# Kernel optimization log

Measured on AMD Instinct MI355X. Metric: run time of the kernel, lower is better.

Reference implementation:

```python
import jax, jax.numpy as jnp
import numpy as np

DIM = 96
GS = 8          # group_size (window side)
CS = 64         # cluster_size
TOPK = 3


def setup_inputs() -> dict:
    key = jax.random.key(0)
    ks = jax.random.split(key, 12)
    B, C, H, W = 4, DIM, 256, 256
    s = 0.02
    return {
        "x":      jax.random.normal(ks[0], (B, C, H, W), jnp.float32),
        "Wq":     jax.random.normal(ks[1], (C, C), jnp.float32) * s,
        "bq":     jnp.zeros((C,), jnp.float32),
        "Wk":     jax.random.normal(ks[2], (C, C), jnp.float32) * s,
        "bk":     jnp.zeros((C,), jnp.float32),
        "Wv":     jax.random.normal(ks[3], (C, C), jnp.float32) * s,
        "bv":     jnp.zeros((C,), jnp.float32),
        "Wp":     jax.random.normal(ks[4], (C, C), jnp.float32) * s,
        "bp":     jnp.zeros((C,), jnp.float32),
        "lepe_w": jax.random.normal(ks[5], (C, 1, 3, 3), jnp.float32) * s,
        "lepe_b": jnp.zeros((C,), jnp.float32),
    }


def _dwconv3x3(x, w, b):
    # x: [N,C,h,w], w: [C,1,3,3] depthwise
    y = jax.lax.conv_general_dilated(
        x, w, window_strides=(1, 1), padding=((1, 1), (1, 1)),
        feature_group_count=x.shape[1],
        dimension_numbers=("NCHW", "OIHW", "NCHW"))
    return y + b[None, :, None, None]


def reference(x, Wq, bq, Wk, bk, Wv, bv, Wp, bp, lepe_w, lepe_b):
    B, C, H, W = x.shape
    gh, gw = H // GS, W // GS
    N = B * gh * gw                      # total windows
    itr = N // CS                        # number of clusters
    P = GS * GS                          # tokens per window
    scale = C ** (-0.5)

    # adaptive_max_pool2d to (gh,gw) == non-overlapping max pool of stride GS
    dsx = x.reshape(B, C, gh, GS, gw, GS).max(axis=(3, 5))        # [B,C,gh,gw]
    dsx = dsx.transpose(0, 2, 3, 1).reshape(itr, CS, C)           # [itr,CS,C]

    # global window-similarity with two-stage topk (faithful to nested loop)
    sim = jnp.einsum('icd,jed->icje', dsx, dsx)                   # [itr,CS,itr,CS]
    blk_s, blk_i = jax.lax.top_k(sim, TOPK)                       # [itr,CS,itr,TOPK]
    blk_gi = blk_i + (jnp.arange(itr) * CS)[None, None, :, None]  # global indices
    cat_s = blk_s.reshape(itr, CS, itr * TOPK)
    cat_i = blk_gi.reshape(itr, CS, itr * TOPK)
    fin_s, fi = jax.lax.top_k(cat_s, TOPK)                        # [itr,CS,TOPK]
    fin_i = jnp.take_along_axis(cat_i, fi, axis=-1)
    sim_score = fin_s.reshape(N, TOPK)
    sim_index = fin_i.reshape(N, TOPK)

    # window partition: [N, P, C]
    xw = x.transpose(0, 2, 3, 1).reshape(B, gh, GS, gw, GS, C)
    xw = xw.transpose(0, 1, 3, 2, 4, 5).reshape(N, P, C)

    # weighted combination of topk neighbor windows
    w = jax.nn.softmax(sim_score, axis=-1)                        # [N,TOPK]
    neighbors = xw[sim_index]                                     # [N,TOPK,P,C]
    context = jnp.einsum('nk,nkpc->npc', w, neighbors)            # [N,P,C]

    # windowed cross attention: Q from x windows, K/V from gathered context
    q = xw @ Wq + bq
    k = context @ Wk + bk
    v = context @ Wv + bv

    # lepe: depthwise conv positional bias on x windows
    x_img = xw.transpose(0, 2, 1).reshape(N, C, GS, GS)
    lepe = _dwconv3x3(x_img, lepe_w, lepe_b).reshape(N, C, P).transpose(0, 2, 1)

    attn = jax.nn.softmax(jnp.einsum('npc,nqc->npq', q, k) * scale, axis=-1)
    out = jnp.einsum('npq,nqc->npc', attn, v) + lepe
    out = out @ Wp + bp                                           # [N,P,C]

    # reverse window partition -> [B,C,H,W]
    out = out.reshape(B, gh, gw, GS, GS, C)
    out = out.transpose(0, 5, 1, 3, 2, 4).reshape(B, C, H, W)
    return out
```

## Files before the change

kernel.cpp:

```cpp
#include <hip/hip_runtime.h>

typedef __attribute__((ext_vector_type(8))) short  short8;
typedef __attribute__((ext_vector_type(4))) float  f32x4;
typedef __attribute__((ext_vector_type(4))) unsigned int uint4v;
typedef __attribute__((ext_vector_type(2))) unsigned int uint2v;

#define NEG_INF (-3.402823466e38f)

__device__ __forceinline__ unsigned short bfbits(float f) {
    unsigned u = __builtin_bit_cast(unsigned, f);
    u += 0x7fffu + ((u >> 16) & 1u);
    return (unsigned short)(u >> 16);
}
__device__ __forceinline__ unsigned pk_bf16(float lo, float hi) {
    return (unsigned)bfbits(lo) | ((unsigned)bfbits(hi) << 16);
}
__device__ __forceinline__ float lofp(unsigned u) {
    return __builtin_bit_cast(float, u << 16);
}
__device__ __forceinline__ float hifp(unsigned u) {
    return __builtin_bit_cast(float, u & 0xffff0000u);
}
__device__ __forceinline__ float bf2f(short x) {
    return __builtin_bit_cast(float, ((unsigned)(unsigned short)x) << 16);
}

__device__ __forceinline__ void ins3(float (&tv)[3], int (&ti)[3], float v, int ci)
{
    if (v > tv[0] || (v == tv[0] && ci < ti[0])) {
        tv[2] = tv[1]; ti[2] = ti[1];
        tv[1] = tv[0]; ti[1] = ti[0];
        tv[0] = v;     ti[0] = ci;
    } else if (v > tv[1] || (v == tv[1] && ci < ti[1])) {
        tv[2] = tv[1]; ti[2] = ti[1];
        tv[1] = v;     ti[1] = ci;
    } else if (v > tv[2] || (v == tv[2] && ci < ti[2])) {
        tv[2] = v;     ti[2] = ci;
    }
}

__global__ __launch_bounds__(256) void k_pool(const float* __restrict__ x,
                                              float* __restrict__ dsxT)
{
    int gid = blockIdx.x * 256 + threadIdx.x;
    int c = gid >> 12;
    int n = gid & 4095;
    int b = n >> 10, i = (n >> 5) & 31, j = n & 31;
    const float* p = x + (((size_t)(b * 96 + c)) << 16) + i * 2048 + j * 8;
    float4 m0 = *(const float4*)p;
    float4 m1 = *(const float4*)(p + 4);
    #pragma unroll
    for (int r = 1; r < 8; ++r) {
        float4 a0 = *(const float4*)(p + r * 256);
        float4 a1 = *(const float4*)(p + r * 256 + 4);
        m0.x = fmaxf(m0.x, a0.x); m0.y = fmaxf(m0.y, a0.y);
        m0.z = fmaxf(m0.z, a0.z); m0.w = fmaxf(m0.w, a0.w);
        m1.x = fmaxf(m1.x, a1.x); m1.y = fmaxf(m1.y, a1.y);
        m1.z = fmaxf(m1.z, a1.z); m1.w = fmaxf(m1.w, a1.w);
    }
    float m = fmaxf(fmaxf(fmaxf(m0.x, m0.y), fmaxf(m0.z, m0.w)),
                    fmaxf(fmaxf(m1.x, m1.y), fmaxf(m1.z, m1.w)));
    dsxT[c * 4096 + n] = m;
}

__global__ __launch_bounds__(768) void k_cast(const float* __restrict__ x,
                                              unsigned short* __restrict__ xwg,
                                              unsigned short* __restrict__ dsxH,
                                              unsigned short* __restrict__ dsxM,
                                              unsigned short* __restrict__ dsxL)
{
    int n = ((blockIdx.x & 7) << 9) | (blockIdx.x >> 3);
    int t = threadIdx.x;
    int cg = t >> 6, p = t & 63;
    int b = n >> 10, i = (n >> 5) & 31, j = n & 31;
    int h = i * 8 + (p >> 3), w = j * 8 + (p & 7);
    size_t base = (((size_t)(b * 96 + 8 * cg)) << 16) + (size_t)(h * 256 + w);
    float v[8];
    #pragma unroll
    for (int jj = 0; jj < 8; ++jj) v[jj] = x[base + (((size_t)jj) << 16)];
    uint4v pk;
    #pragma unroll
    for (int jj = 0; jj < 4; ++jj) pk[jj] = pk_bf16(v[2 * jj], v[2 * jj + 1]);
    *(uint4v*)&xwg[(size_t)n * 6144 + p * 96 + 8 * cg] = pk;
    #pragma unroll
    for (int jj = 0; jj < 8; ++jj) {
        float m = v[jj];
        #pragma unroll
        for (int d = 1; d < 64; d <<= 1) m = fmaxf(m, __shfl_xor(m, d, 64));
        if (p == 0) {
            unsigned short hb = bfbits(m);
            float r1 = m - __builtin_bit_cast(float, ((unsigned)hb) << 16);
            unsigned short mb = bfbits(r1);
            float r2 = r1 - __builtin_bit_cast(float, ((unsigned)mb) << 16);
            dsxH[n * 96 + 8 * cg + jj] = hb;
            dsxM[n * 96 + 8 * cg + jj] = mb;
            dsxL[n * 96 + 8 * cg + jj] = bfbits(r2);
        }
    }
}

__global__ __launch_bounds__(256) void k_sim(const float* __restrict__ dsxT,
                                             float* __restrict__ pv,
                                             int* __restrict__ pi)
{
    __shared__ __align__(16) float qt[32 * 128];
    __shared__ __align__(16) float ct[32 * 144];
    int t = threadIdx.x;
    int qti = blockIdx.x >> 4;
    int ch  = blockIdx.x & 15;
    int ty = t >> 4, tx = t & 15;
    int qb = qti * 128;

    float tv[8][3]; int ti[8][3];
    #pragma unroll
    for (int a = 0; a < 8; ++a)
        #pragma unroll
        for (int k = 0; k < 3; ++k) { tv[a][k] = NEG_INF; ti[a][k] = 0x7fffffff; }

    #pragma unroll
    for (int pass = 0; pass < 2; ++pass) {
        int cb = ch * 256 + pass * 128;
        float acc[8][8];
        #pragma unroll
        for (int a = 0; a < 8; ++a)
            #pragma unroll
            for (int e = 0; e < 8; ++e) acc[a][e] = 0.f;

        for (int kc = 0; kc < 3; ++kc) {
            __syncthreads();
            #pragma unroll
            for (int f4 = 0; f4 < 4; ++f4) {
                int f = t + f4 * 256;
                int kk = f >> 5, cq = f & 31;
                *(float4*)&qt[kk * 128 + 4 * cq] =
                    *(const float4*)&dsxT[(kc * 32 + kk) * 4096 + qb + 4 * cq];
                *(float4*)&ct[kk * 144 + 4 * cq + 4 * (cq >> 3)] =
                    *(const float4*)&dsxT[(kc * 32 + kk) * 4096 + cb + 4 * cq];
            }
            __syncthreads();
            #pragma unroll 2
            for (int kk = 0; kk < 32; ++kk) {
                float4 q0 = *(float4*)&qt[kk * 128 + 8 * ty];
                float4 q1 = *(float4*)&qt[kk * 128 + 8 * ty + 4];
                int e0 = 8 * tx, e1 = 8 * tx + 4;
                float4 c0 = *(float4*)&ct[kk * 144 + e0 + 4 * (e0 >> 5)];
                float4 c1 = *(float4*)&ct[kk * 144 + e1 + 4 * (e1 >> 5)];
                float qv[8] = {q0.x, q0.y, q0.z, q0.w, q1.x, q1.y, q1.z, q1.w};
                float cv[8] = {c0.x, c0.y, c0.z, c0.w, c1.x, c1.y, c1.z, c1.w};
                #pragma unroll
                for (int a = 0; a < 8; ++a)
                    #pragma unroll
                    for (int e = 0; e < 8; ++e)
                        acc[a][e] = fmaf(qv[a], cv[e], acc[a][e]);
            }
        }
        #pragma unroll
        for (int e = 0; e < 8; ++e) {
            int ci = cb + 8 * tx + e;
            #pragma unroll
            for (int a = 0; a < 8; ++a) ins3(tv[a], ti[a], acc[a][e], ci);
        }
    }

    #pragma unroll
    for (int d = 1; d < 16; d <<= 1) {
        #pragma unroll
        for (int a = 0; a < 8; ++a) {
            float ov[3]; int oi[3];
            #pragma unroll
            for (int k = 0; k < 3; ++k) {
                ov[k] = __shfl_xor(tv[a][k], d, 16);
                oi[k] = __shfl_xor(ti[a][k], d, 16);
            }
            #pragma unroll
            for (int k = 0; k < 3; ++k) ins3(tv[a], ti[a], ov[k], oi[k]);
        }
    }
    if (tx == 0) {
        #pragma unroll
        for (int a = 0; a < 8; ++a) {
            int nq = qti * 128 + 8 * ty + a;
            #pragma unroll
            for (int k = 0; k < 3; ++k) {
                pv[nq * 48 + ch * 3 + k] = tv[a][k];
                pi[nq * 48 + ch * 3 + k] = ti[a][k];
            }
        }
    }
}

__global__ __launch_bounds__(256) void k_sim_bf(const unsigned short* __restrict__ dsxH,
                                                const unsigned short* __restrict__ dsxM,
                                                const unsigned short* __restrict__ dsxL,
                                                int* __restrict__ pi)
{
    int t = threadIdx.x;
    int qti = blockIdx.x >> 4;
    int ch  = blockIdx.x & 15;
    int lane = t & 63, wv = t >> 6;
    int l15 = lane & 15, quad = lane >> 4;
    int cb = ch * 256;

    #pragma unroll
    for (int a2 = 0; a2 < 2; ++a2) {
        int at = wv * 2 + a2;
        int qrow = qti * 128 + at * 16 + l15;
        short8 aH[3], aM[3], aL[3];
        #pragma unroll
        for (int ks = 0; ks < 3; ++ks) {
            aH[ks] = *(const short8*)&dsxH[qrow * 96 + ks * 32 + quad * 8];
            aM[ks] = *(const short8*)&dsxM[qrow * 96 + ks * 32 + quad * 8];
            aL[ks] = *(const short8*)&dsxL[qrow * 96 + ks * 32 + quad * 8];
        }
        float tv[4][3]; int ti[4][3];
        #pragma unroll
        for (int r = 0; r < 4; ++r)
            #pragma unroll
            for (int k = 0; k < 3; ++k) { tv[r][k] = NEG_INF; ti[r][k] = 0x7fffffff; }

        for (int bt = 0; bt < 16; ++bt) {
            int crow = cb + bt * 16 + l15;
            f32x4 c  = {0.f, 0.f, 0.f, 0.f};
            f32x4 c2 = {0.f, 0.f, 0.f, 0.f};
            #pragma unroll
            for (int ks = 0; ks < 3; ++ks) {
                short8 bH = *(const short8*)&dsxH[crow * 96 + ks * 32 + quad * 8];
                short8 bM = *(const short8*)&dsxM[crow * 96 + ks * 32 + quad * 8];
                short8 bL = *(const short8*)&dsxL[crow * 96 + ks * 32 + quad * 8];
                c  = __builtin_amdgcn_mfma_f32_16x16x32_bf16(aH[ks], bH, c,  0, 0, 0);
                c2 = __builtin_amdgcn_mfma_f32_16x16x32_bf16(aH[ks], bM, c2, 0, 0, 0);
                c2 = __builtin_amdgcn_mfma_f32_16x16x32_bf16(aM[ks], bH, c2, 0, 0, 0);
                c2 = __builtin_amdgcn_mfma_f32_16x16x32_bf16(aM[ks], bM, c2, 0, 0, 0);
                c2 = __builtin_amdgcn_mfma_f32_16x16x32_bf16(aH[ks], bL, c2, 0, 0, 0);
                c2 = __builtin_amdgcn_mfma_f32_16x16x32_bf16(aL[ks], bH, c2, 0, 0, 0);
            }
            #pragma unroll
            for (int r = 0; r < 4; ++r)
                ins3(tv[r], ti[r], c[r] + c2[r], cb + bt * 16 + l15);
        }
        #pragma unroll
        for (int d = 1; d < 16; d <<= 1) {
            #pragma unroll
            for (int r = 0; r < 4; ++r) {
                float ov[3]; int oi[3];
                #pragma unroll
                for (int k = 0; k < 3; ++k) {
                    ov[k] = __shfl_xor(tv[r][k], d, 16);
                    oi[k] = __shfl_xor(ti[r][k], d, 16);
                }
                #pragma unroll
                for (int k = 0; k < 3; ++k) ins3(tv[r], ti[r], ov[k], oi[k]);
            }
        }
        if (l15 == 0) {
            #pragma unroll
            for (int r = 0; r < 4; ++r) {
                int nq = qti * 128 + at * 16 + quad * 4 + r;
                #pragma unroll
                for (int k = 0; k < 3; ++k)
                    pi[nq * 48 + ch * 3 + k] = ti[r][k];
            }
        }
    }
}

__global__ __launch_bounds__(256) void k_top3x(const unsigned short* __restrict__ dsxH,
                                               const unsigned short* __restrict__ dsxM,
                                               const unsigned short* __restrict__ dsxL,
                                               const int* __restrict__ pi,
                                               float* __restrict__ w3,
                                               int* __restrict__ i3)
{
    int t = threadIdx.x;
    int lane = t & 63, wv = t >> 6;
    int n = blockIdx.x * 4 + wv;
    int cand = (lane < 48) ? pi[n * 48 + lane] : 0;
    float s = 0.f;
    #pragma unroll
    for (int ck = 0; ck < 12; ++ck) {
        short8 qh = *(const short8*)&dsxH[n * 96 + ck * 8];
        short8 qm = *(const short8*)&dsxM[n * 96 + ck * 8];
        short8 ql = *(const short8*)&dsxL[n * 96 + ck * 8];
        short8 kh = *(const short8*)&dsxH[cand * 96 + ck * 8];
        short8 km = *(const short8*)&dsxM[cand * 96 + ck * 8];
        short8 kl = *(const short8*)&dsxL[cand * 96 + ck * 8];
        #pragma unroll
        for (int e = 0; e < 8; ++e) {
            float qv = (bf2f(qh[e]) + bf2f(qm[e])) + bf2f(ql[e]);
            float kv = (bf2f(kh[e]) + bf2f(km[e])) + bf2f(kl[e]);
            s = fmaf(qv, kv, s);
        }
    }
    float tv[3] = {NEG_INF, NEG_INF, NEG_INF};
    int   ti[3] = {0x7fffffff, 0x7fffffff, 0x7fffffff};
    if (lane < 48) { tv[0] = s; ti[0] = cand; }
    #pragma unroll
    for (int d = 1; d < 64; d <<= 1) {
        float ov[3]; int oi[3];
        #pragma unroll
        for (int k = 0; k < 3; ++k) {
            ov[k] = __shfl_xor(tv[k], d, 64);
            oi[k] = __shfl_xor(ti[k], d, 64);
        }
        #pragma unroll
        for (int k = 0; k < 3; ++k) ins3(tv, ti, ov[k], oi[k]);
    }
    if (lane == 0) {
        float e1 = expf(tv[1] - tv[0]);
        float e2 = expf(tv[2] - tv[0]);
        float inv = 1.f / (1.f + e1 + e2);
        w3[n * 3 + 0] = inv;
        w3[n * 3 + 1] = e1 * inv;
        w3[n * 3 + 2] = e2 * inv;
        i3[n * 3 + 0] = ti[0];
        i3[n * 3 + 1] = ti[1];
        i3[n * 3 + 2] = ti[2];
    }
}

__global__ __launch_bounds__(256) void k_topk(const float* __restrict__ pv,
                                              const int* __restrict__ pi,
                                              float* __restrict__ w3,
                                              int* __restrict__ i3)
{
    int n = blockIdx.x * 256 + threadIdx.x;
    float bv[3] = {NEG_INF, NEG_INF, NEG_INF};
    int   bi[3] = {0x7fffffff, 0x7fffffff, 0x7fffffff};
    for (int e = 0; e < 48; ++e)
        ins3(bv, bi, pv[n * 48 + e], pi[n * 48 + e]);
    float e1 = expf(bv[1] - bv[0]);
    float e2 = expf(bv[2] - bv[0]);
    float inv = 1.f / (1.f + e1 + e2);
    w3[n * 3 + 0] = inv;
    w3[n * 3 + 1] = e1 * inv;
    w3[n * 3 + 2] = e2 * inv;
    i3[n * 3 + 0] = bi[0];
    i3[n * 3 + 1] = bi[1];
    i3[n * 3 + 2] = bi[2];
}

__global__ __launch_bounds__(256) void k_prep(const float* __restrict__ Wq,
                                              const float* __restrict__ Wk,
                                              const float* __restrict__ Wv,
                                              const float* __restrict__ Wp,
                                              const float* __restrict__ lw,
                                              unsigned short* __restrict__ WtT,
                                              float* __restrict__ lwT)
{
    int g = blockIdx.x * 256 + threadIdx.x;
    if (g < 4608) {
        int w  = g / 1152;
        int co = (g % 1152) / 12;
        int cg = g % 12;
        const float* src = (w == 0) ? Wq : (w == 1) ? Wk : (w == 2) ? Wv : Wp;
        unsigned short* dst = WtT + w * 9216 + co * 96 + 8 * cg;
        #pragma unroll
        for (int j = 0; j < 8; ++j) dst[j] = bfbits(src[(8 * cg + j) * 96 + co]);
    } else if (g < 5472) {
        int i2 = g - 4608;
        int tap = i2 / 96, c = i2 % 96;
        lwT[tap * 96 + c] = lw[c * 9 + tap];
    }
}

__device__ __forceinline__ size_t win_off(int m)
{
    return (((size_t)(m >> 10) * 96) << 16) +
           (size_t)(((m >> 5) & 31) * 2048 + (m & 31) * 8);
}

__device__ __forceinline__ void gemm_g(const short8* af,
                                       const unsigned short* __restrict__ Wt,
                                       int l15, int quad, f32x4* acc)
{
    #pragma unroll
    for (int nt = 0; nt < 6; ++nt) {
        f32x4 c = {0.f, 0.f, 0.f, 0.f};
        #pragma unroll
        for (int ks = 0; ks < 3; ++ks) {
            short8 bf = *(const short8*)&Wt[(nt * 16 + l15) * 96 + ks * 32 + quad * 8];
            c = __builtin_amdgcn_mfma_f32_16x16x32_bf16(af[ks], bf, c, 0, 0, 0);
        }
        acc[nt] = c;
    }
}

template<bool XWG>
__global__ __attribute__((amdgpu_waves_per_eu(4, 4)))
__launch_bounds__(256) void k_attn(
    const float* __restrict__ x,
    const unsigned short* __restrict__ xwg,
    const unsigned short* __restrict__ WtT,
    const float* __restrict__ lwT,
    const float* __restrict__ bq, const float* __restrict__ bk,
    const float* __restrict__ bv, const float* __restrict__ bp,
    const float* __restrict__ lb,
    const float* __restrict__ w3, const int* __restrict__ i3,
    float* __restrict__ out)
{
    extern __shared__ __align__(16) unsigned short sm[];
    unsigned short* buf1 = sm;
    unsigned short* buf2 = sm + 6656;
    unsigned short* Vt   = sm + 13312;

    int t = threadIdx.x;
    int n = ((blockIdx.x & 7) << 9) | (blockIdx.x >> 3);
    int lane = t & 63, mt = t >> 6;
    int l15 = lane & 15, quad = lane >> 4;

    float wk0 = w3[n * 3 + 0], wk1 = w3[n * 3 + 1], wk2 = w3[n * 3 + 2];
    int   m0  = i3[n * 3 + 0], m1 = i3[n * 3 + 1], m2 = i3[n * 3 + 2];

    if (XWG) {
        #pragma unroll
        for (int it = 0; it < 3; ++it) {
            int g = it * 256 + t;
            int p = g / 12, cg = g % 12;
            int o = p * 96 + 8 * cg;
            uint4v sv = *(const uint4v*)&xwg[(size_t)n * 6144 + o];
            *(uint4v*)&buf1[p * 104 + 8 * cg] = sv;
            uint4v a0 = *(const uint4v*)&xwg[(size_t)m0 * 6144 + o];
            uint4v a1 = *(const uint4v*)&xwg[(size_t)m1 * 6144 + o];
            uint4v a2 = *(const uint4v*)&xwg[(size_t)m2 * 6144 + o];
            uint4v rs;
            #pragma unroll
            for (int e = 0; e < 4; ++e) {
                float lo = wk0 * lofp(a0[e]) + wk1 * lofp(a1[e]) + wk2 * lofp(a2[e]);
                float hi = wk0 * hifp(a0[e]) + wk1 * hifp(a1[e]) + wk2 * hifp(a2[e]);
                rs[e] = pk_bf16(lo, hi);
            }
            *(uint4v*)&buf2[p * 104 + 8 * cg] = rs;
        }
    } else {
        size_t so = win_off(n), o0 = win_off(m0), o1 = win_off(m1), o2 = win_off(m2);
        #pragma unroll
        for (int it = 0; it < 3; ++it) {
            int g = it * 256 + t;
            int p = g / 12, cg = g % 12;
            size_t po = (size_t)((p >> 3) * 256 + (p & 7));
            uint4v ra, rb;
            #pragma unroll
            for (int jj = 0; jj < 4; ++jj) {
                size_t clo = (((size_t)(8 * cg + 2 * jj)) << 16) + po;
                size_t chi = clo + ((size_t)1 << 16);
                ra[jj] = pk_bf16(x[so + clo], x[so + chi]);
                float blo = wk0 * x[o0 + clo] + wk1 * x[o1 + clo] + wk2 * x[o2 + clo];
                float bhi = wk0 * x[o0 + chi] + wk1 * x[o1 + chi] + wk2 * x[o2 + chi];
                rb[jj] = pk_bf16(blo, bhi);
            }
            *(uint4v*)&buf1[p * 104 + 8 * cg] = ra;
            *(uint4v*)&buf2[p * 104 + 8 * cg] = rb;
        }
    }
    __syncthreads();

    short8 af_a[3], af_b[3];
    int arow = (mt * 16 + l15) * 104;
    #pragma unroll
    for (int ks = 0; ks < 3; ++ks) {
        af_a[ks] = *(const short8*)&buf1[arow + ks * 32 + quad * 8];
        af_b[ks] = *(const short8*)&buf2[arow + ks * 32 + quad * 8];
    }
    unsigned Lp[12];
    {
        int rowp = mt * 16 + l15;
        int c0 = 24 * quad;
        int rr0 = rowp >> 3, ss0 = rowp & 7;
        float lac[24];
        #pragma unroll
        for (int q4 = 0; q4 < 6; ++q4) {
            float4 bb = *(const float4*)&lb[c0 + 4 * q4];
            lac[4 * q4] = bb.x; lac[4 * q4 + 1] = bb.y;
            lac[4 * q4 + 2] = bb.z; lac[4 * q4 + 3] = bb.w;
        }
        #pragma unroll
        for (int dr = -1; dr <= 1; ++dr) {
            int rr = rr0 + dr;
            if ((unsigned)rr >= 8u) continue;
            #pragma unroll
            for (int dss = -1; dss <= 1; ++dss) {
                int ss = ss0 + dss;
                if ((unsigned)ss >= 8u) continue;
                int pp = rr * 8 + ss;
                int tap = (dr + 1) * 3 + (dss + 1);
                const uint4v* ap = (const uint4v*)&buf1[pp * 104 + c0];
                uint4v av0 = ap[0], av1 = ap[1], av2 = ap[2];
                float wf[24];
                #pragma unroll
                for (int q4 = 0; q4 < 6; ++q4) {
                    float4 ww = *(const float4*)&lwT[tap * 96 + c0 + 4 * q4];
                    wf[4 * q4] = ww.x; wf[4 * q4 + 1] = ww.y;
                    wf[4 * q4 + 2] = ww.z; wf[4 * q4 + 3] = ww.w;
                }
                #pragma unroll
                for (int u = 0; u < 12; ++u) {
                    unsigned uu = (u < 4) ? av0[u] : (u < 8) ? av1[u - 4] : av2[u - 8];
                    lac[2 * u]     = fmaf(wf[2 * u],     lofp(uu), lac[2 * u]);
                    lac[2 * u + 1] = fmaf(wf[2 * u + 1], hifp(uu), lac[2 * u + 1]);
                }
            }
        }
        #pragma unroll
        for (int u = 0; u < 12; ++u) Lp[u] = pk_bf16(lac[2 * u], lac[2 * u + 1]);
    }
    __syncthreads();

    {
        f32x4 qa[6];
        gemm_g(af_a, WtT, l15, quad, qa);
        #pragma unroll
        for (int nt = 0; nt < 6; ++nt) {
            int col = nt * 16 + l15;
            float bb = bq[col];
            #pragma unroll
            for (int r = 0; r < 4; ++r)
                buf1[(mt * 16 + quad * 4 + r) * 104 + col] = bfbits(qa[nt][r] + bb);
        }
    }
    __builtin_amdgcn_sched_barrier(0);
    {
        f32x4 ka[6];
        gemm_g(af_b, WtT + 9216, l15, quad, ka);
        #pragma unroll
        for (int nt = 0; nt < 6; ++nt) {
            int col = nt * 16 + l15;
            float bb = bk[col];
            #pragma unroll
            for (int r = 0; r < 4; ++r)
                buf2[(mt * 16 + quad * 4 + r) * 104 + col] = bfbits(ka[nt][r] + bb);
        }
    }
    __builtin_amdgcn_sched_barrier(0);
    {
        f32x4 va[6];
        gemm_g(af_b, WtT + 18432, l15, quad, va);
        #pragma unroll
        for (int nt = 0; nt < 6; ++nt) {
            float bb = bv[nt * 16 + l15];
            uint2v pk;
            pk[0] = pk_bf16(va[nt][0] + bb, va[nt][1] + bb);
            pk[1] = pk_bf16(va[nt][2] + bb, va[nt][3] + bb);
            *(uint2v*)&Vt[(nt * 16 + l15) * 72 + mt * 16 + quad * 4] = pk;
        }
    }
    __syncthreads();

    float pr[4][4], inv4[4];
    {
        short8 qf[3];
        #pragma unroll
        for (int ks = 0; ks < 3; ++ks)
            qf[ks] = *(const short8*)&buf1[arow + ks * 32 + quad * 8];
        f32x4 sa[4];
        #pragma unroll
        for (int nt = 0; nt < 4; ++nt) {
            f32x4 c = {0.f, 0.f, 0.f, 0.f};
            #pragma unroll
            for (int ks = 0; ks < 3; ++ks) {
                short8 bf = *(const short8*)&buf2[(nt * 16 + l15) * 104 + ks * 32 + quad * 8];
                c = __builtin_amdgcn_mfma_f32_16x16x32_bf16(qf[ks], bf, c, 0, 0, 0);
            }
            sa[nt] = c;
        }
        const float scale = 0.10206207261596575f;
        #pragma unroll
        for (int r = 0; r < 4; ++r) {
            float mx = fmaxf(fmaxf(sa[0][r], sa[1][r]), fmaxf(sa[2][r], sa[3][r]));
            #pragma unroll
            for (int d = 1; d < 16; d <<= 1) mx = fmaxf(mx, __shfl_xor(mx, d, 16));
            float sum = 0.f;
            #pragma unroll
            for (int nt = 0; nt < 4; ++nt) {
                float e = __expf((sa[nt][r] - mx) * scale);
                pr[r][nt] = e; sum += e;
            }
            #pragma unroll
            for (int d = 1; d < 16; d <<= 1) sum += __shfl_xor(sum, d, 16);
            inv4[r] = 1.f / sum;
        }
    }
    __syncthreads();

    #pragma unroll
    for (int r = 0; r < 4; ++r) {
        #pragma unroll
        for (int nt = 0; nt < 4; ++nt)
            buf1[(mt * 16 + quad * 4 + r) * 104 + nt * 16 + l15] =
                bfbits(pr[r][nt] * inv4[r]);
    }
    {
        uint4v* lp = (uint4v*)&buf2[arow + 24 * quad];
        uint4v l0 = {Lp[0], Lp[1], Lp[2], Lp[3]};
        uint4v l1 = {Lp[4], Lp[5], Lp[6], Lp[7]};
        uint4v l2 = {Lp[8], Lp[9], Lp[10], Lp[11]};
        lp[0] = l0; lp[1] = l1; lp[2] = l2;
    }

    {
        short8 sf[2];
        sf[0] = *(const short8*)&buf1[arow + quad * 8];
        sf[1] = *(const short8*)&buf1[arow + 32 + quad * 8];
        f32x4 oa[6];
        #pragma unroll
        for (int nt = 0; nt < 6; ++nt) {
            f32x4 c = {0.f, 0.f, 0.f, 0.f};
            #pragma unroll
            for (int ks = 0; ks < 2; ++ks) {
                short8 bf = *(const short8*)&Vt[(nt * 16 + l15) * 72 + ks * 32 + quad * 8];
                c = __builtin_amdgcn_mfma_f32_16x16x32_bf16(sf[ks], bf, c, 0, 0, 0);
            }
            oa[nt] = c;
        }
        #pragma unroll
        for (int nt = 0; nt < 6; ++nt)
            #pragma unroll
            for (int r = 0; r < 4; ++r)
                buf1[(mt * 16 + quad * 4 + r) * 104 + nt * 16 + l15] = bfbits(oa[nt][r]);
    }

    {
        short8 of[3], lf[3];
        #pragma unroll
        for (int ks = 0; ks < 3; ++ks) {
            of[ks] = *(const short8*)&buf1[arow + ks * 32 + quad * 8];
            lf[ks] = *(const short8*)&buf2[arow + ks * 32 + quad * 8];
        }
        const unsigned short* Wp_ = WtT + 27648;
        int b = n >> 10, ii = (n >> 5) & 31, jj = n & 31;
        size_t pbase = (size_t)(ii * 2048 + jj * 8 + mt * 512 +
                                (quad >> 1) * 256 + (quad & 1) * 4);
        #pragma unroll
        for (int nt = 0; nt < 6; ++nt) {
            f32x4 c = {0.f, 0.f, 0.f, 0.f};
            #pragma unroll
            for (int ks = 0; ks < 3; ++ks) {
                short8 bf = *(const short8*)&Wp_[(nt * 16 + l15) * 96 + ks * 32 + quad * 8];
                c = __builtin_amdgcn_mfma_f32_16x16x32_bf16(of[ks], bf, c, 0, 0, 0);
                c = __builtin_amdgcn_mfma_f32_16x16x32_bf16(lf[ks], bf, c, 0, 0, 0);
            }
            int co = nt * 16 + l15;
            float bb = bp[co];
            float4 st;
            st.x = c[0] + bb; st.y = c[1] + bb; st.z = c[2] + bb; st.w = c[3] + bb;
            *(float4*)&out[(((size_t)(b * 96 + co)) << 16) + pbase] = st;
        }
    }
}

extern "C" void kernel_launch(void* const* d_in, const int* in_sizes, int n_in,
                              void* d_out, int out_size, void* d_ws, size_t ws_size,
                              hipStream_t stream)
{
    (void)in_sizes; (void)n_in; (void)out_size;
    const float* x  = (const float*)d_in[0];
    const float* Wq = (const float*)d_in[1];
    const float* bq = (const float*)d_in[2];
    const float* Wk = (const float*)d_in[3];
    const float* bk = (const float*)d_in[4];
    const float* Wv = (const float*)d_in[5];
    const float* bv = (const float*)d_in[6];
    const float* Wp = (const float*)d_in[7];
    const float* bp = (const float*)d_in[8];
    const float* lw = (const float*)d_in[9];
    const float* lb = (const float*)d_in[10];
    float* out = (float*)d_out;

    char* ws = (char*)d_ws;
    float* dsxT = (float*)ws;
    unsigned short* dsxH = (unsigned short*)ws;
    unsigned short* dsxM = (unsigned short*)(ws + 786432);
    unsigned short* dsxL = (unsigned short*)(ws + 1572864);
    float* pv   = (float*)(ws + 1572864);
    int*   pi   = (int*)  (ws + 2359296);
    float* w3   = (float*)(ws + 3145728);
    int*   i3   = (int*)  (ws + 3194880);
    unsigned short* WtT = (unsigned short*)(ws + 3244032);
    float* lwT  = (float*)(ws + 3317760);
    unsigned short* xwg = (unsigned short*)(ws + 3321344);
    bool use_xwg = (ws_size >= 53652992ull);

    (void)hipFuncSetAttribute(reinterpret_cast<const void*>(&k_attn<true>),
                        hipFuncAttributeMaxDynamicSharedMemorySize, 40448);
    (void)hipFuncSetAttribute(reinterpret_cast<const void*>(&k_attn<false>),
                        hipFuncAttributeMaxDynamicSharedMemorySize, 40448);

    k_prep<<<22, 256, 0, stream>>>(Wq, Wk, Wv, Wp, lw, WtT, lwT);
    if (use_xwg) {
        k_cast<<<4096, 768, 0, stream>>>(x, xwg, dsxH, dsxM, dsxL);
        k_sim_bf<<<512, 256, 0, stream>>>(dsxH, dsxM, dsxL, pi);
        k_top3x<<<1024, 256, 0, stream>>>(dsxH, dsxM, dsxL, pi, w3, i3);
        k_attn<true><<<4096, 256, 40448, stream>>>(x, xwg, WtT, lwT, bq, bk, bv, bp,
                                                   lb, w3, i3, out);
    } else {
        k_pool<<<1536, 256, 0, stream>>>(x, dsxT);
        k_sim<<<512, 256, 0, stream>>>(dsxT, pv, pi);
        k_topk<<<16, 256, 0, stream>>>(pv, pi, w3, i3);
        k_attn<false><<<4096, 256, 40448, stream>>>(x, nullptr, WtT, lwT, bq, bk, bv, bp,
                                                    lb, w3, i3, out);
    }
}
```

Measured before the change: 428.4 us.

## Stage similarity B tiles through double-buffered LDS and raise MFMA wave priority

The similarity kernel now has each block cover 64 query rows instead of 128 and launches twice as many blocks. The three bf16 key planes are staged cooperatively into a double-buffered shared-memory tile, with the next tile's global loads issued before the current tile's MFMAs. This replaces redundant per-wave global loads of B and overlaps them with compute. Separately, s_setprio is raised around the MFMA loops in the attention kernel to favour matrix-issuing waves, at the cost of an extra barrier per tile and more LDS use.

```diff
diff --git a/kernel.cpp b/kernel.cpp
--- a/kernel.cpp
+++ b/kernel.cpp
@@ -189,11 +189,12 @@
     }
 }
 
-__global__ __launch_bounds__(256) void k_sim_bf(const unsigned short* __restrict__ dsxH,
-                                                const unsigned short* __restrict__ dsxM,
-                                                const unsigned short* __restrict__ dsxL,
-                                                int* __restrict__ pi)
-{
+__global__ __launch_bounds__(256, 4) void k_sim_bf(const unsigned short* __restrict__ dsxH,
+                                                   const unsigned short* __restrict__ dsxM,
+                                                   const unsigned short* __restrict__ dsxL,
+                                                   int* __restrict__ pi)
+{
+    __shared__ __align__(16) unsigned short Bs[2][16 * 296];
     int t = threadIdx.x;
     int qti = blockIdx.x >> 4;
     int ch  = blockIdx.x & 15;
@@ -201,65 +202,103 @@
     int l15 = lane & 15, quad = lane >> 4;
     int cb = ch * 256;
 
-    #pragma unroll
-    for (int a2 = 0; a2 < 2; ++a2) {
-        int at = wv * 2 + a2;
-        int qrow = qti * 128 + at * 16 + l15;
-        short8 aH[3], aM[3], aL[3];
+    int qrow = qti * 64 + wv * 16 + l15;
+    short8 aH[3], aM[3], aL[3];
+    #pragma unroll
+    for (int ks = 0; ks < 3; ++ks) {
+        aH[ks] = *(const short8*)&dsxH[qrow * 96 + ks * 32 + quad * 8];
+        aM[ks] = *(const short8*)&dsxM[qrow * 96 + ks * 32 + quad * 8];
+        aL[ks] = *(const short8*)&dsxL[qrow * 96 + ks * 32 + quad * 8];
+    }
+
+    int ldsoff[3], goff[3];
+    const unsigned short* srcp[3];
+    #pragma unroll
+    for (int kc = 0; kc < 3; ++kc) {
+        int c = t + kc * 256;
+        int row = c / 36, w36 = c % 36;
+        int plane = w36 / 12, idx = w36 % 12;
+        ldsoff[kc] = row * 296 + plane * 96 + idx * 8;
+        goff[kc]   = row * 96 + idx * 8;
+        srcp[kc]   = (plane == 0) ? dsxH : (plane == 1) ? dsxM : dsxL;
+    }
+    bool third = (t < 64);
+
+    float tv[4][3]; int ti[4][3];
+    #pragma unroll
+    for (int r = 0; r < 4; ++r)
+        #pragma unroll
+        for (int k = 0; k < 3; ++k) { tv[r][k] = NEG_INF; ti[r][k] = 0x7fffffff; }
+
+    {
+        int base = cb * 96;
+        uint4v v0 = *(const uint4v*)&srcp[0][base + goff[0]];
+        uint4v v1 = *(const uint4v*)&srcp[1][base + goff[1]];
+        *(uint4v*)&Bs[0][ldsoff[0]] = v0;
+        *(uint4v*)&Bs[0][ldsoff[1]] = v1;
+        if (third) {
+            uint4v v2 = *(const uint4v*)&srcp[2][base + goff[2]];
+            *(uint4v*)&Bs[0][ldsoff[2]] = v2;
+        }
+    }
+    __syncthreads();
+
+    for (int st = 0; st < 16; ++st) {
+        int cur = st & 1;
+        uint4v p0, p1, p2;
+        if (st < 15) {
+            int base = (cb + (st + 1) * 16) * 96;
+            p0 = *(const uint4v*)&srcp[0][base + goff[0]];
+            p1 = *(const uint4v*)&srcp[1][base + goff[1]];
+            if (third) p2 = *(const uint4v*)&srcp[2][base + goff[2]];
+        }
+        f32x4 c = {0.f, 0.f, 0.f, 0.f};
+        f32x4 c2 = {0.f, 0.f, 0.f, 0.f};
         #pragma unroll
         for (int ks = 0; ks < 3; ++ks) {
-            aH[ks] = *(const short8*)&dsxH[qrow * 96 + ks * 32 + quad * 8];
-            aM[ks] = *(const short8*)&dsxM[qrow * 96 + ks * 32 + quad * 8];
-            aL[ks] = *(const short8*)&dsxL[qrow * 96 + ks * 32 + quad * 8];
-        }
-        float tv[4][3]; int ti[4][3];
+            int bo = l15 * 296 + ks * 32 + quad * 8;
+            short8 bH = *(const short8*)&Bs[cur][bo];
+            short8 bM = *(const short8*)&Bs[cur][bo + 96];
+            short8 bL = *(const short8*)&Bs[cur][bo + 192];
+            c  = __builtin_amdgcn_mfma_f32_16x16x32_bf16(aH[ks], bH, c,  0, 0, 0);
+            c2 = __builtin_amdgcn_mfma_f32_16x16x32_bf16(aH[ks], bM, c2, 0, 0, 0);
+            c2 = __builtin_amdgcn_mfma_f32_16x16x32_bf16(aM[ks], bH, c2, 0, 0, 0);
+            c2 = __builtin_amdgcn_mfma_f32_16x16x32_bf16(aM[ks], bM, c2, 0, 0, 0);
+            c2 = __builtin_amdgcn_mfma_f32_16x16x32_bf16(aH[ks], bL, c2, 0, 0, 0);
+            c2 = __builtin_amdgcn_mfma_f32_16x16x32_bf16(aL[ks], bH, c2, 0, 0, 0);
+        }
         #pragma unroll
         for (int r = 0; r < 4; ++r)
-            #pragma unroll
-            for (int k = 0; k < 3; ++k) { tv[r][k] = NEG_INF; ti[r][k] = 0x7fffffff; }
-
-        for (int bt = 0; bt < 16; ++bt) {
-            int crow = cb + bt * 16 + l15;
-            f32x4 c  = {0.f, 0.f, 0.f, 0.f};
-            f32x4 c2 = {0.f, 0.f, 0.f, 0.f};
-            #pragma unroll
-            for (int ks = 0; ks < 3; ++ks) {
-                short8 bH = *(const short8*)&dsxH[crow * 96 + ks * 32 + quad * 8];
-                short8 bM = *(const short8*)&dsxM[crow * 96 + ks * 32 + quad * 8];
-                short8 bL = *(const short8*)&dsxL[crow * 96 + ks * 32 + quad * 8];
-                c  = __builtin_amdgcn_mfma_f32_16x16x32_bf16(aH[ks], bH, c,  0, 0, 0);
-                c2 = __builtin_amdgcn_mfma_f32_16x16x32_bf16(aH[ks], bM, c2, 0, 0, 0);
-                c2 = __builtin_amdgcn_mfma_f32_16x16x32_bf16(aM[ks], bH, c2, 0, 0, 0);
-                c2 = __builtin_amdgcn_mfma_f32_16x16x32_bf16(aM[ks], bM, c2, 0, 0, 0);
-                c2 = __builtin_amdgcn_mfma_f32_16x16x32_bf16(aH[ks], bL, c2, 0, 0, 0);
-                c2 = __builtin_amdgcn_mfma_f32_16x16x32_bf16(aL[ks], bH, c2, 0, 0, 0);
-            }
-            #pragma unroll
-            for (int r = 0; r < 4; ++r)
-                ins3(tv[r], ti[r], c[r] + c2[r], cb + bt * 16 + l15);
-        }
-        #pragma unroll
-        for (int d = 1; d < 16; d <<= 1) {
-            #pragma unroll
-            for (int r = 0; r < 4; ++r) {
-                float ov[3]; int oi[3];
-                #pragma unroll
-                for (int k = 0; k < 3; ++k) {
-                    ov[k] = __shfl_xor(tv[r][k], d, 16);
-                    oi[k] = __shfl_xor(ti[r][k], d, 16);
-                }
-                #pragma unroll
-                for (int k = 0; k < 3; ++k) ins3(tv[r], ti[r], ov[k], oi[k]);
-            }
-        }
-        if (l15 == 0) {
-            #pragma unroll
-            for (int r = 0; r < 4; ++r) {
-                int nq = qti * 128 + at * 16 + quad * 4 + r;
-                #pragma unroll
-                for (int k = 0; k < 3; ++k)
-                    pi[nq * 48 + ch * 3 + k] = ti[r][k];
-            }
+            ins3(tv[r], ti[r], c[r] + c2[r], cb + st * 16 + l15);
+        if (st < 15) {
+            *(uint4v*)&Bs[cur ^ 1][ldsoff[0]] = p0;
+            *(uint4v*)&Bs[cur ^ 1][ldsoff[1]] = p1;
+            if (third) *(uint4v*)&Bs[cur ^ 1][ldsoff[2]] = p2;
+        }
+        __syncthreads();
+    }
+
+    #pragma unroll
+    for (int d = 1; d < 16; d <<= 1) {
+        #pragma unroll
+        for (int r = 0; r < 4; ++r) {
+            float ov[3]; int oi[3];
+            #pragma unroll
+            for (int k = 0; k < 3; ++k) {
+                ov[k] = __shfl_xor(tv[r][k], d, 16);
+                oi[k] = __shfl_xor(ti[r][k], d, 16);
+            }
+            #pragma unroll
+            for (int k = 0; k < 3; ++k) ins3(tv[r], ti[r], ov[k], oi[k]);
+        }
+    }
+    if (l15 == 0) {
+        #pragma unroll
+        for (int r = 0; r < 4; ++r) {
+            int nq = qti * 64 + wv * 16 + quad * 4 + r;
+            #pragma unroll
+            for (int k = 0; k < 3; ++k)
+                pi[nq * 48 + ch * 3 + k] = ti[r][k];
         }
     }
 }
@@ -373,6 +412,7 @@
                                        const unsigned short* __restrict__ Wt,
                                        int l15, int quad, f32x4* acc)
 {
+    __builtin_amdgcn_s_setprio(1);
     #pragma unroll
     for (int nt = 0; nt < 6; ++nt) {
         f32x4 c = {0.f, 0.f, 0.f, 0.f};
@@ -383,6 +423,7 @@
         }
         acc[nt] = c;
     }
+    __builtin_amdgcn_s_setprio(0);
 }
 
 template<bool XWG>
@@ -552,6 +593,7 @@
         for (int ks = 0; ks < 3; ++ks)
             qf[ks] = *(const short8*)&buf1[arow + ks * 32 + quad * 8];
         f32x4 sa[4];
+        __builtin_amdgcn_s_setprio(1);
         #pragma unroll
         for (int nt = 0; nt < 4; ++nt) {
             f32x4 c = {0.f, 0.f, 0.f, 0.f};
@@ -562,6 +604,7 @@
             }
             sa[nt] = c;
         }
+        __builtin_amdgcn_s_setprio(0);
         const float scale = 0.10206207261596575f;
         #pragma unroll
         for (int r = 0; r < 4; ++r) {
@@ -601,6 +644,7 @@
         sf[0] = *(const short8*)&buf1[arow + quad * 8];
         sf[1] = *(const short8*)&buf1[arow + 32 + quad * 8];
         f32x4 oa[6];
+        __builtin_amdgcn_s_setprio(1);
         #pragma unroll
         for (int nt = 0; nt < 6; ++nt) {
             f32x4 c = {0.f, 0.f, 0.f, 0.f};
@@ -611,6 +655,7 @@
             }
             oa[nt] = c;
         }
+        __builtin_amdgcn_s_setprio(0);
         #pragma unroll
         for (int nt = 0; nt < 6; ++nt)
             #pragma unroll
@@ -629,6 +674,7 @@
         int b = n >> 10, ii = (n >> 5) & 31, jj = n & 31;
         size_t pbase = (size_t)(ii * 2048 + jj * 8 + mt * 512 +
                                 (quad >> 1) * 256 + (quad & 1) * 4);
+        __builtin_amdgcn_s_setprio(1);
         #pragma unroll
         for (int nt = 0; nt < 6; ++nt) {
             f32x4 c = {0.f, 0.f, 0.f, 0.f};
@@ -644,6 +690,7 @@
             st.x = c[0] + bb; st.y = c[1] + bb; st.z = c[2] + bb; st.w = c[3] + bb;
             *(float4*)&out[(((size_t)(b * 96 + co)) << 16) + pbase] = st;
         }
+        __builtin_amdgcn_s_setprio(0);
     }
 }
 
@@ -687,7 +734,7 @@
     k_prep<<<22, 256, 0, stream>>>(Wq, Wk, Wv, Wp, lw, WtT, lwT);
     if (use_xwg) {
         k_cast<<<4096, 768, 0, stream>>>(x, xwg, dsxH, dsxM, dsxL);
-        k_sim_bf<<<512, 256, 0, stream>>>(dsxH, dsxM, dsxL, pi);
+        k_sim_bf<<<1024, 256, 0, stream>>>(dsxH, dsxM, dsxL, pi);
         k_top3x<<<1024, 256, 0, stream>>>(dsxH, dsxM, dsxL, pi, w3, i3);
         k_attn<true><<<4096, 256, 40448, stream>>>(x, xwg, WtT, lwT, bq, bk, bv, bp,
                                                    lb, w3, i3, out);
```

After: 396.3 us. -7.5%, faster.
